# Kernel optimization log

Hardware: AMD Instinct MI355X
Metric: run time of the kernel (lower is better)

## Reference

```python
import jax, jax.numpy as jnp
import numpy as np

EPS = 1e-5

def _normalize(v):
    # F.normalize(v, p=2, dim=-1, eps=1e-5): v / max(||v||_2, eps)
    n = jnp.sqrt(jnp.sum(v * v, axis=-1, keepdims=True))
    return v / jnp.maximum(n, EPS)

def setup_inputs() -> dict:
    key = jax.random.key(0)
    kx, ke = jax.random.split(key)
    B, T, C, K = 16, 2048, 512, 1024
    x = jax.random.normal(kx, (B, T, C), dtype=jnp.float32)
    emb = jax.random.normal(ke, (K, C), dtype=jnp.float32)  # embedding.weight
    return {"x": x, "emb": emb}

def reference(x, emb):
    B, T, C = x.shape
    # Squared distances (argmin of cdist == argmin of squared distance):
    x2 = jnp.sum(x * x, axis=-1, keepdims=True)          # [B,T,1]
    e2 = jnp.sum(emb * emb, axis=-1)                      # [K]
    xe = jnp.einsum('btc,kc->btk', x, emb)                # [B,T,K]
    dist2 = x2 - 2.0 * xe + e2                            # [B,T,K]
    idx = jnp.argmin(dist2, axis=-1)                      # [B,T] int
    quant = jnp.take(emb, idx, axis=0)                    # [B,T,C]
    x_norm = _normalize(x)
    q_norm = _normalize(quant)
    commitment_loss = jnp.mean((jax.lax.stop_gradient(q_norm) - x_norm) ** 2, axis=(1, 2))  # [B]
    codebook_loss = jnp.mean((q_norm - jax.lax.stop_gradient(x_norm)) ** 2, axis=(1, 2))    # [B]
    # Straight-through estimator
    quant_out = x + jax.lax.stop_gradient(quant - x)
    return quant_out, codebook_loss, commitment_loss, idx
```

## Files before the change

kernel.cpp:

```cpp
#include <hip/hip_runtime.h>

typedef unsigned short u16;
typedef unsigned int u32;
typedef _Float16 half8 __attribute__((ext_vector_type(8)));
typedef float f32x4 __attribute__((ext_vector_type(4)));

#define BT    32768
#define CD    512
#define KC    1024
#define LOFF1 16777216
#define LOFF2 16777232
#define IOFF  16777248

#define WS_EH   0
#define WS_E2   1048576
#define WS_PART 1052672

static __device__ __forceinline__ u16 f2h(float f) {
  union { _Float16 h; u16 u; } c;
  c.h = (_Float16)f;
  return c.u;
}

__global__ __launch_bounds__(256) void conve_kernel(const float* __restrict__ emb,
                                                    u16* __restrict__ eh,
                                                    float* __restrict__ e2) {
  const int lane = threadIdx.x & 63;
  const int r    = blockIdx.x * 4 + (threadIdx.x >> 6);
  const float4* er = reinterpret_cast<const float4*>(emb + (size_t)r * CD);
  const float4 a = er[lane*2], b = er[lane*2+1];
  uint4 o;
  o.x = (u32)f2h(a.x) | ((u32)f2h(a.y) << 16);
  o.y = (u32)f2h(a.z) | ((u32)f2h(a.w) << 16);
  o.z = (u32)f2h(b.x) | ((u32)f2h(b.y) << 16);
  o.w = (u32)f2h(b.z) | ((u32)f2h(b.w) << 16);
  const int gt = r >> 4, lm = r & 15;
  const int ks = lane >> 2, lq = lane & 3;
  reinterpret_cast<uint4*>(eh)[(gt*64 + ks*4 + lq)*16 + lm] = o;
  float s = a.x*a.x + a.y*a.y + a.z*a.z + a.w*a.w
          + b.x*b.x + b.y*b.y + b.z*b.z + b.w*b.w;
  for (int off = 32; off > 0; off >>= 1) s += __shfl_down(s, off, 64);
  if (lane == 0) e2[r] = s;
}

__global__ __launch_bounds__(512) void mfma_fused_kernel(
    const u16* __restrict__ eh, const float* __restrict__ e2,
    const float* __restrict__ x, const float* __restrict__ emb,
    float* __restrict__ out, float* __restrict__ part) {
  __shared__ __align__(16) char smem[70144];
  u16*    sA    = (u16*)smem;
  float*  e2s   = (float*)(smem + 65536);
  int*    win   = (int*)(smem + 69632);
  u32*    cand  = (u32*)smem;
  int*    top4k = (int*)(smem + 65536);
  double* dref  = (double*)smem;
  float*  q2a   = (float*)(smem + 2048);
  float*  xqa   = (float*)(smem + 3072);
  float*  x2a   = (float*)(smem + 4096);

  const int tid  = threadIdx.x;
  const int wv   = tid >> 6;
  const int lane = tid & 63;
  const int lm   = lane & 15;
  const int lq   = lane >> 4;
  const int m0   = blockIdx.x * 64;

  const u16* eB = eh + wv*16384 + lane*8;

  half8 afA[4], afB[4], bfA[2], bfB[2];

#define PREF(IT, AF, BF) do {                                        \
    const int nt_ = (IT) >> 4, ks_ = (IT) & 15;                      \
    const u16* pb_ = eB + nt_ * 131072 + ks_ * 512;                  \
    BF[0] = *(const half8*)(pb_);                                    \
    BF[1] = *(const half8*)(pb_ + 8192);                             \
    const u16* pa_ = sA + ks_ * 512 + lane * 8;                      \
    AF[0] = *(const half8*)(pa_);                                    \
    AF[1] = *(const half8*)(pa_ + 8192);                             \
    AF[2] = *(const half8*)(pa_ + 16384);                            \
    AF[3] = *(const half8*)(pa_ + 24576);                            \
  } while (0)

#define MM(AF, BF) do {                                              \
    _Pragma("unroll") for (int ti_ = 0; ti_ < 4; ++ti_)              \
      _Pragma("unroll") for (int tj_ = 0; tj_ < 2; ++tj_)            \
        acc[ti_][tj_] = __builtin_amdgcn_mfma_f32_16x16x32_f16(      \
            AF[ti_], BF[tj_], acc[ti_][tj_], 0, 0, 0);               \
  } while (0)

#define FOLD(NT) do {                                                \
    _Pragma("unroll") for (int tj_ = 0; tj_ < 2; ++tj_) {            \
      const int col_ = (NT)*256 + wv*32 + tj_*16 + lm;               \
      const float ek_ = e2s[col_];                                   \
      _Pragma("unroll") for (int ti_ = 0; ti_ < 4; ++ti_)            \
        _Pragma("unroll") for (int rg_ = 0; rg_ < 4; ++rg_) {        \
          const float d_ = ek_ - 2.f * acc[ti_][tj_][rg_] + 1024.f;  \
          const u32 p_ = (__float_as_uint(d_) & 0xFFFFFC00u) | (u32)col_; \
          const int s_ = ti_*4 + rg_;                                \
          if (p_ < t0[s_]) { t1[s_] = t0[s_]; t0[s_] = p_; }         \
          else if (p_ < t1[s_]) { t1[s_] = p_; }                     \
          acc[ti_][tj_][rg_] = 0.f;                                  \
        }                                                            \
    }                                                                \
  } while (0)

  {
    const float* xb = x + (size_t)m0 * CD;
    const int tl = tid & 15;
    const int tc = tid >> 4;
#pragma unroll 4
    for (int i = 0; i < 16; ++i) {
      const int r  = (i & 3) * 16 + tl;
      const int c4 = tc * 4 + (i >> 2);
      const float4 v = *(const float4*)(xb + (size_t)r * CD + c4 * 4);
      const int ks  = c4 >> 3;
      const int lqw = (c4 >> 1) & 3;
      const int j   = (c4 & 1) << 2;
      const int ti  = r >> 4, lmw = r & 15;
      uint2 o;
      o.x = (u32)f2h(v.x) | ((u32)f2h(v.y) << 16);
      o.y = (u32)f2h(v.z) | ((u32)f2h(v.w) << 16);
      *(uint2*)(sA + ((ti*16 + ks) << 9) + ((lqw << 4) + lmw) * 8 + j) = o;
    }
    e2s[tid]       = e2[tid];
    e2s[tid + 512] = e2[tid + 512];
  }
  __syncthreads();

  f32x4 acc[4][2];
#pragma unroll
  for (int i = 0; i < 4; ++i)
#pragma unroll
    for (int j = 0; j < 2; ++j)
      acc[i][j] = (f32x4){0.f, 0.f, 0.f, 0.f};

  u32 t0[16], t1[16];
#pragma unroll
  for (int s = 0; s < 16; ++s) { t0[s] = 0xFFFFFFFFu; t1[s] = 0xFFFFFFFFu; }

  PREF(0, afA, bfA);

#pragma unroll 1
  for (int itp = 0; itp < 32; ++itp) {
    const int it = itp << 1;
    PREF(it + 1, afB, bfB);
    MM(afA, bfA);
    if (itp != 31) PREF(it + 2, afA, bfA);
    MM(afB, bfB);
    if ((itp & 7) == 7) FOLD(itp >> 3);
  }
#undef PREF
#undef MM
#undef FOLD

  __syncthreads();
#pragma unroll
  for (int s = 0; s < 16; ++s) {
    const int ti = s >> 2, reg = s & 3;
    const int row = ti*16 + lq*4 + reg;
    uint2 pr; pr.x = t0[s]; pr.y = t1[s];
    *reinterpret_cast<uint2*>(&cand[row*256 + wv*32 + lm*2]) = pr;
  }
  __syncthreads();

  if (tid < 64) {
    u32 u0 = 0xFFFFFFFFu, u1 = 0xFFFFFFFFu, u2 = 0xFFFFFFFFu, u3 = 0xFFFFFFFFu;
    for (int i = 0; i < 256; ++i) {
      const u32 v = cand[tid*256 + ((i + tid*4) & 255)];
      if (v < u3) {
        if (v < u2) {
          u3 = u2;
          if (v < u1) {
            u2 = u1;
            if (v < u0) { u1 = u0; u0 = v; } else { u1 = v; }
          } else { u2 = v; }
        } else { u3 = v; }
      }
    }
    top4k[tid*4+0] = (int)(u0 & 1023u);
    top4k[tid*4+1] = (int)(u1 & 1023u);
    top4k[tid*4+2] = (int)(u2 & 1023u);
    top4k[tid*4+3] = (int)(u3 & 1023u);
  }
  __syncthreads();

  if (tid < 256) {
    const int rr = tid >> 2, cc = tid & 3;
    const int k = top4k[rr*4 + cc];
    const float4* xr = reinterpret_cast<const float4*>(x   + (size_t)(m0+rr) * CD);
    const float4* er = reinterpret_cast<const float4*>(emb + (size_t)k * CD);
    double d0 = 0.0, d1 = 0.0;
    float q2 = 0.f, xq = 0.f, x2 = 0.f;
    for (int i = 0; i < CD/4; ++i) {
      const float4 a = xr[i], b = er[i];
      const double ta = (double)a.x - (double)b.x;
      const double tb = (double)a.y - (double)b.y;
      const double tc = (double)a.z - (double)b.z;
      const double td = (double)a.w - (double)b.w;
      d0 += ta*ta + tc*tc;
      d1 += tb*tb + td*td;
      q2 += b.x*b.x + b.y*b.y + b.z*b.z + b.w*b.w;
      xq += a.x*b.x + a.y*b.y + a.z*b.z + a.w*b.w;
      x2 += a.x*a.x + a.y*a.y + a.z*a.z + a.w*a.w;
    }
    dref[rr*4 + cc] = d0 + d1;
    q2a[rr*4 + cc] = q2;
    xqa[rr*4 + cc] = xq;
    if (cc == 0) x2a[rr] = x2;
  }
  __syncthreads();

  if (tid < 64) {
    double bd = dref[tid*4]; int bk = top4k[tid*4]; int bc = 0;
#pragma unroll
    for (int c = 1; c < 4; ++c) {
      const double dc = dref[tid*4 + c];
      const int kc = top4k[tid*4 + c];
      if (dc < bd || (dc == bd && kc < bk)) { bd = dc; bk = kc; bc = c; }
    }
    const int gr = m0 + tid;
    out[IOFF + gr] = (float)bk;
    win[tid] = bk;

    const float q2 = q2a[tid*4 + bc];
    const float xq = xqa[tid*4 + bc];
    const float x2 = x2a[tid];
    const float nx = fmaxf(sqrtf(x2), 1e-5f);
    const float nq = fmaxf(sqrtf(q2), 1e-5f);
    float s = q2/(nq*nq) + x2/(nx*nx) - 2.f*xq/(nx*nq);
    for (int off = 32; off > 0; off >>= 1) s += __shfl_down(s, off, 64);
    if (tid == 0) part[blockIdx.x] = s;
  }
  __syncthreads();

  {
    const float4* e4 = reinterpret_cast<const float4*>(emb);
    float4* ob4 = reinterpret_cast<float4*>(out + (size_t)m0 * CD);
#pragma unroll 4
    for (int i = 0; i < 16; ++i) {
      const int f = tid + (i << 9);
      const int k = win[f >> 7];
      ob4[f] = e4[k*128 + (f & 127)];
    }
  }
}

__global__ void loss_write_kernel(const float* __restrict__ part,
                                  float* __restrict__ out) {
  const int t = threadIdx.x;
  if (t < 16) {
    float acc = 0.f;
    for (int i = 0; i < 32; ++i) acc += part[32*t + i];
    const float v = acc * (1.f / 1048576.f);
    out[LOFF1 + t] = v;
    out[LOFF2 + t] = v;
  }
}

extern "C" void kernel_launch(void* const* d_in, const int* in_sizes, int n_in,
                              void* d_out, int out_size, void* d_ws, size_t ws_size,
                              hipStream_t stream) {
  const float* x   = (const float*)d_in[0];
  const float* emb = (const float*)d_in[1];
  float* out = (float*)d_out;

  u16*   eh   = (u16*)((char*)d_ws + WS_EH);
  float* e2   = (float*)((char*)d_ws + WS_E2);
  float* part = (float*)((char*)d_ws + WS_PART);

  conve_kernel<<<KC / 4, 256, 0, stream>>>(emb, eh, e2);
  mfma_fused_kernel<<<BT / 64, 512, 0, stream>>>(eh, e2, x, emb, out, part);
  loss_write_kernel<<<1, 64, 0, stream>>>(part, out);
}
```

Before: 207.9 us.

## Double rows per block to 128 and restructure MFMA loop with setprio

Each block now processes 128 rows instead of 64. This halves the grid and halves how often the fp16 codebook is streamed from global memory, since each B fragment now feeds twice as many MFMAs. The inner loop is restructured so A fragments are reloaded from LDS per half-tile, B fragments are double-buffered from global, and MFMA groups are wrapped in s_setprio. The cost is doubled LDS (about 135KB, limiting the CU to one block), twice as many accumulator and top-2 registers, and fewer blocks (256) to spread across the CUs.

```diff
diff --git a/kernel.cpp b/kernel.cpp
--- a/kernel.cpp
+++ b/kernel.cpp
@@ -47,52 +47,55 @@
     const u16* __restrict__ eh, const float* __restrict__ e2,
     const float* __restrict__ x, const float* __restrict__ emb,
     float* __restrict__ out, float* __restrict__ part) {
-  __shared__ __align__(16) char smem[70144];
+  __shared__ __align__(16) char smem[135680];
   u16*    sA    = (u16*)smem;
-  float*  e2s   = (float*)(smem + 65536);
-  int*    win   = (int*)(smem + 69632);
+  float*  e2s   = (float*)(smem + 131072);
+  int*    win   = (int*)(smem + 135168);
   u32*    cand  = (u32*)smem;
-  int*    top4k = (int*)(smem + 65536);
+  int*    top4k = (int*)(smem + 131072);
   double* dref  = (double*)smem;
-  float*  q2a   = (float*)(smem + 2048);
-  float*  xqa   = (float*)(smem + 3072);
-  float*  x2a   = (float*)(smem + 4096);
+  float*  q2a   = (float*)(smem + 4096);
+  float*  xqa   = (float*)(smem + 6144);
+  float*  x2a   = (float*)(smem + 8192);
 
   const int tid  = threadIdx.x;
   const int wv   = tid >> 6;
   const int lane = tid & 63;
   const int lm   = lane & 15;
   const int lq   = lane >> 4;
-  const int m0   = blockIdx.x * 64;
+  const int m0   = blockIdx.x * 128;
 
   const u16* eB = eh + wv*16384 + lane*8;
 
-  half8 afA[4], afB[4], bfA[2], bfB[2];
-
-#define PREF(IT, AF, BF) do {                                        \
+  half8 af[4], bf[2][2];
+
+#define BLOAD(IT, BF) do {                                           \
     const int nt_ = (IT) >> 4, ks_ = (IT) & 15;                      \
     const u16* pb_ = eB + nt_ * 131072 + ks_ * 512;                  \
     BF[0] = *(const half8*)(pb_);                                    \
     BF[1] = *(const half8*)(pb_ + 8192);                             \
-    const u16* pa_ = sA + ks_ * 512 + lane * 8;                      \
-    AF[0] = *(const half8*)(pa_);                                    \
-    AF[1] = *(const half8*)(pa_ + 8192);                             \
-    AF[2] = *(const half8*)(pa_ + 16384);                            \
-    AF[3] = *(const half8*)(pa_ + 24576);                            \
-  } while (0)
-
-#define MM(AF, BF) do {                                              \
+  } while (0)
+
+#define ALOADH(IT, H) do {                                           \
+    const u16* pa_ = sA + ((IT) & 15) * 512 + (H) * 32768 + lane * 8;\
+    af[0] = *(const half8*)(pa_);                                    \
+    af[1] = *(const half8*)(pa_ + 8192);                             \
+    af[2] = *(const half8*)(pa_ + 16384);                            \
+    af[3] = *(const half8*)(pa_ + 24576);                            \
+  } while (0)
+
+#define MMH(BF, H) do {                                              \
     _Pragma("unroll") for (int ti_ = 0; ti_ < 4; ++ti_)              \
       _Pragma("unroll") for (int tj_ = 0; tj_ < 2; ++tj_)            \
-        acc[ti_][tj_] = __builtin_amdgcn_mfma_f32_16x16x32_f16(      \
-            AF[ti_], BF[tj_], acc[ti_][tj_], 0, 0, 0);               \
+        acc[(H)*4 + ti_][tj_] = __builtin_amdgcn_mfma_f32_16x16x32_f16( \
+            af[ti_], BF[tj_], acc[(H)*4 + ti_][tj_], 0, 0, 0);       \
   } while (0)
 
 #define FOLD(NT) do {                                                \
     _Pragma("unroll") for (int tj_ = 0; tj_ < 2; ++tj_) {            \
       const int col_ = (NT)*256 + wv*32 + tj_*16 + lm;               \
       const float ek_ = e2s[col_];                                   \
-      _Pragma("unroll") for (int ti_ = 0; ti_ < 4; ++ti_)            \
+      _Pragma("unroll") for (int ti_ = 0; ti_ < 8; ++ti_)            \
         _Pragma("unroll") for (int rg_ = 0; rg_ < 4; ++rg_) {        \
           const float d_ = ek_ - 2.f * acc[ti_][tj_][rg_] + 1024.f;  \
           const u32 p_ = (__float_as_uint(d_) & 0xFFFFFC00u) | (u32)col_; \
@@ -104,14 +107,16 @@
     }                                                                \
   } while (0)
 
+  BLOAD(0, bf[0]); BLOAD(1, bf[1]);
+
   {
     const float* xb = x + (size_t)m0 * CD;
     const int tl = tid & 15;
     const int tc = tid >> 4;
 #pragma unroll 4
-    for (int i = 0; i < 16; ++i) {
-      const int r  = (i & 3) * 16 + tl;
-      const int c4 = tc * 4 + (i >> 2);
+    for (int i = 0; i < 32; ++i) {
+      const int r  = (i & 7) * 16 + tl;
+      const int c4 = tc * 4 + (i >> 3);
       const float4 v = *(const float4*)(xb + (size_t)r * CD + c4 * 4);
       const int ks  = c4 >> 3;
       const int lqw = (c4 >> 1) & 3;
@@ -127,35 +132,42 @@
   }
   __syncthreads();
 
-  f32x4 acc[4][2];
-#pragma unroll
-  for (int i = 0; i < 4; ++i)
+  f32x4 acc[8][2];
+#pragma unroll
+  for (int i = 0; i < 8; ++i)
 #pragma unroll
     for (int j = 0; j < 2; ++j)
       acc[i][j] = (f32x4){0.f, 0.f, 0.f, 0.f};
 
-  u32 t0[16], t1[16];
-#pragma unroll
-  for (int s = 0; s < 16; ++s) { t0[s] = 0xFFFFFFFFu; t1[s] = 0xFFFFFFFFu; }
-
-  PREF(0, afA, bfA);
+  u32 t0[32], t1[32];
+#pragma unroll
+  for (int s = 0; s < 32; ++s) { t0[s] = 0xFFFFFFFFu; t1[s] = 0xFFFFFFFFu; }
 
 #pragma unroll 1
-  for (int itp = 0; itp < 32; ++itp) {
-    const int it = itp << 1;
-    PREF(it + 1, afB, bfB);
-    MM(afA, bfA);
-    if (itp != 31) PREF(it + 2, afA, bfA);
-    MM(afB, bfB);
-    if ((itp & 7) == 7) FOLD(itp >> 3);
-  }
-#undef PREF
-#undef MM
+  for (int nt = 0; nt < 4; ++nt) {
+#pragma unroll
+    for (int b = 0; b < 16; ++b) {
+      const int it = nt * 16 + b;
+      ALOADH(it, 0);
+      __builtin_amdgcn_s_setprio(1);
+      MMH(bf[b & 1], 0);
+      __builtin_amdgcn_s_setprio(0);
+      ALOADH(it, 1);
+      __builtin_amdgcn_s_setprio(1);
+      MMH(bf[b & 1], 1);
+      __builtin_amdgcn_s_setprio(0);
+      BLOAD(it + 2, bf[b & 1]);
+    }
+    FOLD(nt);
+  }
+#undef BLOAD
+#undef ALOADH
+#undef MMH
 #undef FOLD
 
   __syncthreads();
 #pragma unroll
-  for (int s = 0; s < 16; ++s) {
+  for (int s = 0; s < 32; ++s) {
     const int ti = s >> 2, reg = s & 3;
     const int row = ti*16 + lq*4 + reg;
     uint2 pr; pr.x = t0[s]; pr.y = t1[s];
@@ -163,10 +175,10 @@
   }
   __syncthreads();
 
-  if (tid < 64) {
+  if (tid < 128) {
     u32 u0 = 0xFFFFFFFFu, u1 = 0xFFFFFFFFu, u2 = 0xFFFFFFFFu, u3 = 0xFFFFFFFFu;
     for (int i = 0; i < 256; ++i) {
-      const u32 v = cand[tid*256 + ((i + tid*4) & 255)];
+      const u32 v = cand[tid*256 + ((i + tid*2) & 255)];
       if (v < u3) {
         if (v < u2) {
           u3 = u2;
@@ -184,7 +196,7 @@
   }
   __syncthreads();
 
-  if (tid < 256) {
+  {
     const int rr = tid >> 2, cc = tid & 3;
     const int k = top4k[rr*4 + cc];
     const float4* xr = reinterpret_cast<const float4*>(x   + (size_t)(m0+rr) * CD);
@@ -210,7 +222,7 @@
   }
   __syncthreads();
 
-  if (tid < 64) {
+  if (tid < 128) {
     double bd = dref[tid*4]; int bk = top4k[tid*4]; int bc = 0;
 #pragma unroll
     for (int c = 1; c < 4; ++c) {
@@ -229,7 +241,7 @@
     const float nq = fmaxf(sqrtf(q2), 1e-5f);
     float s = q2/(nq*nq) + x2/(nx*nx) - 2.f*xq/(nx*nq);
     for (int off = 32; off > 0; off >>= 1) s += __shfl_down(s, off, 64);
-    if (tid == 0) part[blockIdx.x] = s;
+    if (lane == 0) part[blockIdx.x*2 + wv] = s;
   }
   __syncthreads();
 
@@ -237,7 +249,7 @@
     const float4* e4 = reinterpret_cast<const float4*>(emb);
     float4* ob4 = reinterpret_cast<float4*>(out + (size_t)m0 * CD);
 #pragma unroll 4
-    for (int i = 0; i < 16; ++i) {
+    for (int i = 0; i < 32; ++i) {
       const int f = tid + (i << 9);
       const int k = win[f >> 7];
       ob4[f] = e4[k*128 + (f & 127)];
@@ -269,6 +281,6 @@
   float* part = (float*)((char*)d_ws + WS_PART);
 
   conve_kernel<<<KC / 4, 256, 0, stream>>>(emb, eh, e2);
-  mfma_fused_kernel<<<BT / 64, 512, 0, stream>>>(eh, e2, x, emb, out, part);
+  mfma_fused_kernel<<<BT / 128, 512, 0, stream>>>(eh, e2, x, emb, out, part);
   loss_write_kernel<<<1, 64, 0, stream>>>(part, out);
 }
```

Result: slower. 329.4 us (+58.5%).

## Restructure MFMA loop with deeper B prefetch, staggered tiles and setprio

Applied to the files above, without the earlier changes.

Splits the A (LDS) and B (global) fragment loads so the global B fragments are prefetched two iterations ahead. The B loads for the first two iterations are issued before the x-to-LDS staging, so their latency overlaps that setup. Each block starts at a different N-tile (blockIdx & 3) to spread concurrent accesses to the codebook, and the MFMA bursts are raised in wave priority with s_setprio. The inner loop is fully unrolled per N-tile with launch_bounds(512,1). The aim is to hide global load latency and contention, at the cost of more register pressure and code size. BLOAD(it+2) at the last iteration reads past the logical range, but it wraps via &3 and stays in bounds.

```diff
diff --git a/kernel.cpp b/kernel.cpp
--- a/kernel.cpp
+++ b/kernel.cpp
@@ -43,7 +43,7 @@
   if (lane == 0) e2[r] = s;
 }
 
-__global__ __launch_bounds__(512) void mfma_fused_kernel(
+__global__ __launch_bounds__(512, 1) void mfma_fused_kernel(
     const u16* __restrict__ eh, const float* __restrict__ e2,
     const float* __restrict__ x, const float* __restrict__ emb,
     float* __restrict__ out, float* __restrict__ part) {
@@ -64,17 +64,22 @@
   const int lm   = lane & 15;
   const int lq   = lane >> 4;
   const int m0   = blockIdx.x * 64;
+  const int bofs = blockIdx.x & 3;
 
   const u16* eB = eh + wv*16384 + lane*8;
 
-  half8 afA[4], afB[4], bfA[2], bfB[2];
-
-#define PREF(IT, AF, BF) do {                                        \
-    const int nt_ = (IT) >> 4, ks_ = (IT) & 15;                      \
+  half8 afA[4], afB[4], bf[2][2];
+
+#define BLOAD(IT, BF) do {                                           \
+    const int nt_ = ((((IT) >> 4)) + bofs) & 3;                      \
+    const int ks_ = (IT) & 15;                                       \
     const u16* pb_ = eB + nt_ * 131072 + ks_ * 512;                  \
     BF[0] = *(const half8*)(pb_);                                    \
     BF[1] = *(const half8*)(pb_ + 8192);                             \
-    const u16* pa_ = sA + ks_ * 512 + lane * 8;                      \
+  } while (0)
+
+#define ALOAD(IT, AF) do {                                           \
+    const u16* pa_ = sA + ((IT) & 15) * 512 + lane * 8;              \
     AF[0] = *(const half8*)(pa_);                                    \
     AF[1] = *(const half8*)(pa_ + 8192);                             \
     AF[2] = *(const half8*)(pa_ + 16384);                            \
@@ -89,8 +94,9 @@
   } while (0)
 
 #define FOLD(NT) do {                                                \
+    const int nte_ = ((NT) + bofs) & 3;                              \
     _Pragma("unroll") for (int tj_ = 0; tj_ < 2; ++tj_) {            \
-      const int col_ = (NT)*256 + wv*32 + tj_*16 + lm;               \
+      const int col_ = nte_*256 + wv*32 + tj_*16 + lm;               \
       const float ek_ = e2s[col_];                                   \
       _Pragma("unroll") for (int ti_ = 0; ti_ < 4; ++ti_)            \
         _Pragma("unroll") for (int rg_ = 0; rg_ < 4; ++rg_) {        \
@@ -103,6 +109,8 @@
         }                                                            \
     }                                                                \
   } while (0)
+
+  BLOAD(0, bf[0]); BLOAD(1, bf[1]);
 
   {
     const float* xb = x + (size_t)m0 * CD;
@@ -138,18 +146,31 @@
 #pragma unroll
   for (int s = 0; s < 16; ++s) { t0[s] = 0xFFFFFFFFu; t1[s] = 0xFFFFFFFFu; }
 
-  PREF(0, afA, bfA);
+  ALOAD(0, afA);
 
 #pragma unroll 1
-  for (int itp = 0; itp < 32; ++itp) {
-    const int it = itp << 1;
-    PREF(it + 1, afB, bfB);
-    MM(afA, bfA);
-    if (itp != 31) PREF(it + 2, afA, bfA);
-    MM(afB, bfB);
-    if ((itp & 7) == 7) FOLD(itp >> 3);
-  }
-#undef PREF
+  for (int nt = 0; nt < 4; ++nt) {
+#pragma unroll
+    for (int b = 0; b < 16; ++b) {
+      const int it = nt * 16 + b;
+      if ((b & 1) == 0) {
+        ALOAD(it + 1, afB);
+        __builtin_amdgcn_s_setprio(1);
+        MM(afA, bf[0]);
+        __builtin_amdgcn_s_setprio(0);
+        BLOAD(it + 2, bf[0]);
+      } else {
+        ALOAD(it + 1, afA);
+        __builtin_amdgcn_s_setprio(1);
+        MM(afB, bf[1]);
+        __builtin_amdgcn_s_setprio(0);
+        BLOAD(it + 2, bf[1]);
+      }
+    }
+    FOLD(nt);
+  }
+#undef BLOAD
+#undef ALOAD
 #undef MM
 #undef FOLD
 
```

After: 315.7 us. 1.52x slower.

## Split fused MFMA kernel into argmin and separate refine/gather kernel

Applied to the files above, without the earlier changes.

The fused kernel is split in two. The MFMA argmin kernel now only writes the top-4 candidate indices per row to workspace. A new 256-thread refine kernel recomputes exact double-precision distances, picks the winner, computes the loss partials and gathers the output rows. The aim is to keep the heavy-shared-memory MFMA kernel lean, perhaps freeing registers and LDS and shortening its tail, and to let the memory-bound refine/gather stage run with a lighter footprint. The cost is an extra launch and a workspace round-trip for the candidate indices.

```diff
diff --git a/kernel.cpp b/kernel.cpp
--- a/kernel.cpp
+++ b/kernel.cpp
@@ -15,6 +15,7 @@
 #define WS_EH   0
 #define WS_E2   1048576
 #define WS_PART 1052672
+#define WS_TOP4 1056768
 
 static __device__ __forceinline__ u16 f2h(float f) {
   union { _Float16 h; u16 u; } c;
@@ -43,20 +44,14 @@
   if (lane == 0) e2[r] = s;
 }
 
-__global__ __launch_bounds__(512) void mfma_fused_kernel(
+__global__ __launch_bounds__(512) void mfma_argmin_kernel(
     const u16* __restrict__ eh, const float* __restrict__ e2,
-    const float* __restrict__ x, const float* __restrict__ emb,
-    float* __restrict__ out, float* __restrict__ part) {
+    const float* __restrict__ x, int* __restrict__ top4ws) {
   __shared__ __align__(16) char smem[70144];
   u16*    sA    = (u16*)smem;
   float*  e2s   = (float*)(smem + 65536);
-  int*    win   = (int*)(smem + 69632);
   u32*    cand  = (u32*)smem;
   int*    top4k = (int*)(smem + 65536);
-  double* dref  = (double*)smem;
-  float*  q2a   = (float*)(smem + 2048);
-  float*  xqa   = (float*)(smem + 3072);
-  float*  x2a   = (float*)(smem + 4096);
 
   const int tid  = threadIdx.x;
   const int wv   = tid >> 6;
@@ -184,9 +179,27 @@
   }
   __syncthreads();
 
-  if (tid < 256) {
+  if (tid < 256) top4ws[blockIdx.x * 256 + tid] = top4k[tid];
+}
+
+__global__ __launch_bounds__(256) void refine_kernel(
+    const int* __restrict__ top4ws, const float* __restrict__ x,
+    const float* __restrict__ emb, float* __restrict__ out,
+    float* __restrict__ part) {
+  __shared__ double dref[256];
+  __shared__ float  q2a[256];
+  __shared__ float  xqa[256];
+  __shared__ float  x2a[64];
+  __shared__ int    kk[256];
+  __shared__ int    win[64];
+
+  const int tid = threadIdx.x;
+  const int m0  = blockIdx.x * 64;
+
+  {
     const int rr = tid >> 2, cc = tid & 3;
-    const int k = top4k[rr*4 + cc];
+    const int k = top4ws[blockIdx.x * 256 + tid];
+    kk[tid] = k;
     const float4* xr = reinterpret_cast<const float4*>(x   + (size_t)(m0+rr) * CD);
     const float4* er = reinterpret_cast<const float4*>(emb + (size_t)k * CD);
     double d0 = 0.0, d1 = 0.0;
@@ -203,19 +216,19 @@
       xq += a.x*b.x + a.y*b.y + a.z*b.z + a.w*b.w;
       x2 += a.x*a.x + a.y*a.y + a.z*a.z + a.w*a.w;
     }
-    dref[rr*4 + cc] = d0 + d1;
-    q2a[rr*4 + cc] = q2;
-    xqa[rr*4 + cc] = xq;
+    dref[tid] = d0 + d1;
+    q2a[tid] = q2;
+    xqa[tid] = xq;
     if (cc == 0) x2a[rr] = x2;
   }
   __syncthreads();
 
   if (tid < 64) {
-    double bd = dref[tid*4]; int bk = top4k[tid*4]; int bc = 0;
+    double bd = dref[tid*4]; int bk = kk[tid*4]; int bc = 0;
 #pragma unroll
     for (int c = 1; c < 4; ++c) {
       const double dc = dref[tid*4 + c];
-      const int kc = top4k[tid*4 + c];
+      const int kc = kk[tid*4 + c];
       if (dc < bd || (dc == bd && kc < bk)) { bd = dc; bk = kc; bc = c; }
     }
     const int gr = m0 + tid;
@@ -237,8 +250,8 @@
     const float4* e4 = reinterpret_cast<const float4*>(emb);
     float4* ob4 = reinterpret_cast<float4*>(out + (size_t)m0 * CD);
 #pragma unroll 4
-    for (int i = 0; i < 16; ++i) {
-      const int f = tid + (i << 9);
+    for (int i = 0; i < 32; ++i) {
+      const int f = tid + (i << 8);
       const int k = win[f >> 7];
       ob4[f] = e4[k*128 + (f & 127)];
     }
@@ -267,8 +280,10 @@
   u16*   eh   = (u16*)((char*)d_ws + WS_EH);
   float* e2   = (float*)((char*)d_ws + WS_E2);
   float* part = (float*)((char*)d_ws + WS_PART);
+  int*   top4 = (int*)((char*)d_ws + WS_TOP4);
 
   conve_kernel<<<KC / 4, 256, 0, stream>>>(emb, eh, e2);
-  mfma_fused_kernel<<<BT / 64, 512, 0, stream>>>(eh, e2, x, emb, out, part);
+  mfma_argmin_kernel<<<BT / 64, 512, 0, stream>>>(eh, e2, x, top4);
+  refine_kernel<<<BT / 64, 256, 0, stream>>>(top4, x, emb, out, part);
   loss_write_kernel<<<1, 64, 0, stream>>>(part, out);
 }
```

New measurement: 221.8 us. 6.7% more time.
